# Performance work log

Measured on AMD Instinct MI355X. Metric: run time of the kernel, lower is better.

The kernel has to match this reference:

```python
import jax, jax.numpy as jnp
import numpy as np

B, S, IN_DIM, EMBED, H = 2, 2048, 512, 512, 8
HD = EMBED // H


def setup_inputs() -> dict:
    key = jax.random.key(0)
    ks = jax.random.split(key, 6)
    x = jax.random.normal(ks[0], (B, S, IN_DIM), dtype=jnp.float32)
    dist_mat = jax.random.normal(ks[1], (B, H, S, S), dtype=jnp.float32) * 0.02
    path_mat = jax.random.normal(ks[2], (B, H, S, S), dtype=jnp.float32) * 0.02
    # xavier-uniform-style init scale
    qkv_w = jax.random.normal(ks[3], (IN_DIM, 3 * EMBED), dtype=jnp.float32) * (1.0 / np.sqrt(IN_DIM))
    qkv_b = jnp.zeros((3 * EMBED,), dtype=jnp.float32)
    o_w = jax.random.normal(ks[4], (EMBED, EMBED), dtype=jnp.float32) * (1.0 / np.sqrt(EMBED))
    o_b = jnp.zeros((EMBED,), dtype=jnp.float32)
    return {"x": x, "dist_mat": dist_mat, "path_mat": path_mat,
            "qkv_w": qkv_w, "qkv_b": qkv_b, "o_w": o_w, "o_b": o_b}


def reference(x, dist_mat, path_mat, qkv_w, qkv_b, o_w, o_b):
    b, s, _ = x.shape
    qkv = x @ qkv_w + qkv_b                         # [B,S,3*EMBED]
    qkv = qkv.reshape(b, s, H, 3 * HD).transpose(0, 2, 1, 3)  # [B,H,S,3*HD]
    q, k, v = jnp.split(qkv, 3, axis=-1)            # each [B,H,S,HD]
    logits = jnp.einsum('bhqd,bhkd->bhqk', q, k) / jnp.sqrt(jnp.float32(HD))
    attn = jax.nn.softmax(logits, axis=-1)
    attn = attn + dist_mat + path_mat               # post-softmax bias (breaks flash fusion)
    vals = jnp.einsum('bhqk,bhkd->bhqd', attn, v)   # [B,H,S,HD]
    vals = vals.transpose(0, 2, 1, 3).reshape(b, s, EMBED)
    return vals @ o_w + o_b
```

## Files before the change

kernel.cpp:

```cpp
#include <hip/hip_runtime.h>
#include <stdint.h>
#include <stddef.h>

#define B_ 2
#define H_ 8
#define S_ 2048
#define D_ 64
#define E_ 512
#define N3_ 1536
#define M_ (B_*S_)
#define K_ 512

typedef __attribute__((ext_vector_type(4))) float f32x4;
typedef __attribute__((ext_vector_type(8))) __bf16 bf16x8;
typedef __attribute__((ext_vector_type(4))) __bf16 bf16x4;

static __device__ __forceinline__ int swz(int b) { return b ^ (((b >> 7) & 7) << 4); }

static __device__ __forceinline__ void gl_lds16(const void* g, void* l) {
    __builtin_amdgcn_global_load_lds((const __attribute__((address_space(1))) void*)g,
                                     (__attribute__((address_space(3))) void*)l, 16, 0, 0);
}

__global__ void cvt_bf16_kernel(const float* __restrict__ in, __bf16* __restrict__ out, int n4) {
    int i = blockIdx.x * blockDim.x + threadIdx.x;
    if (i < n4) {
        float4 v = reinterpret_cast<const float4*>(in)[i];
        bf16x4 o;
        o[0] = (__bf16)v.x; o[1] = (__bf16)v.y; o[2] = (__bf16)v.z; o[3] = (__bf16)v.w;
        reinterpret_cast<bf16x4*>(out)[i] = o;
    }
}

__global__ void transpose_cvt_kernel(const float* __restrict__ in, __bf16* __restrict__ out,
                                     int R, int C) {
    __shared__ float tile[32][33];
    int tc = blockIdx.x * 32, tr = blockIdx.y * 32;
    int lx = threadIdx.x & 31, ly = threadIdx.x >> 5;
    #pragma unroll
    for (int p = 0; p < 4; ++p) {
        int r = tr + ly + p * 8, c = tc + lx;
        if (r < R && c < C) tile[ly + p * 8][lx] = in[(size_t)r * C + c];
    }
    __syncthreads();
    #pragma unroll
    for (int p = 0; p < 4; ++p) {
        int oc = tc + ly + p * 8;
        int orow = tr + lx;
        if (oc < C && orow < R) out[(size_t)oc * R + orow] = (__bf16)tile[lx][ly + p * 8];
    }
}

__global__ void transpose_v_kernel(const __bf16* __restrict__ v, __bf16* __restrict__ vt) {
    __shared__ __bf16 t[64][65];
    int bh = blockIdx.x >> 5;
    int s0 = (blockIdx.x & 31) << 6;
    int tid = threadIdx.x;
    const __bf16* src = v + ((size_t)bh * S_ + s0) * D_;
    #pragma unroll
    for (int p = 0; p < 2; ++p) {
        int idx = (p * 256 + tid) * 8;
        int r = idx >> 6, c = idx & 63;
        bf16x8 val = *reinterpret_cast<const bf16x8*>(src + (size_t)r * D_ + c);
        #pragma unroll
        for (int e = 0; e < 8; ++e) t[r][c + e] = val[e];
    }
    __syncthreads();
    __bf16* dst = vt + (size_t)bh * D_ * S_ + s0;
    #pragma unroll
    for (int p = 0; p < 16; ++p) {
        int idx = p * 256 + tid;
        int d = idx >> 6, s = idx & 63;
        dst[(size_t)d * S_ + s] = t[s][d];
    }
}

template<int MODE>
__global__ __launch_bounds__(256, 2) void gemm_kernel(
    const __bf16* __restrict__ A, const __bf16* __restrict__ Bt,
    const float* __restrict__ bias,
    void* __restrict__ o0, void* __restrict__ o1, void* __restrict__ o2,
    int M, int N, int K)
{
    __shared__ __align__(16) __bf16 lA[128 * 64];
    __shared__ __align__(16) __bf16 lB[128 * 64];
    const int tid = threadIdx.x;
    const int wave = tid >> 6, lane = tid & 63;
    const int wm = wave >> 1, wn = wave & 1;
    const int m0 = blockIdx.y * 128, n0 = blockIdx.x * 128;
    const int l15 = lane & 15, l4 = lane >> 4;

    f32x4 acc[4][4] = {};

    for (int k0 = 0; k0 < K; k0 += 64) {
        __syncthreads();
        #pragma unroll
        for (int p = 0; p < 4; ++p) {
            int base = p * 4096 + wave * 1024;
            int js = swz(base + lane * 16);
            int row = js >> 7, colb = js & 127;
            gl_lds16((const char*)A + ((size_t)(m0 + row) * K + k0) * 2 + colb, (char*)lA + base);
            gl_lds16((const char*)Bt + ((size_t)(n0 + row) * K + k0) * 2 + colb, (char*)lB + base);
        }
        __syncthreads();
        #pragma unroll
        for (int ks = 0; ks < 2; ++ks) {
            bf16x8 af[4], bfr[4];
            #pragma unroll
            for (int i = 0; i < 4; ++i) {
                af[i]  = *(const bf16x8*)((const char*)lA + swz(((wm * 64 + i * 16 + l15) << 7) + ks * 64 + (l4 << 4)));
                bfr[i] = *(const bf16x8*)((const char*)lB + swz(((wn * 64 + i * 16 + l15) << 7) + ks * 64 + (l4 << 4)));
            }
            #pragma unroll
            for (int i = 0; i < 4; ++i)
                #pragma unroll
                for (int j = 0; j < 4; ++j)
                    acc[i][j] = __builtin_amdgcn_mfma_f32_16x16x32_bf16(af[i], bfr[j], acc[i][j], 0, 0, 0);
        }
    }
    #pragma unroll
    for (int i = 0; i < 4; ++i) {
        int mg0 = m0 + wm * 64 + i * 16 + (l4 << 2);
        #pragma unroll
        for (int j = 0; j < 4; ++j) {
            int ng = n0 + wn * 64 + j * 16 + l15;
            float bv = bias[ng];
            #pragma unroll
            for (int r = 0; r < 4; ++r) {
                int m = mg0 + r;
                float val = acc[i][j][r] + bv;
                if (MODE == 0) {
                    int h = ng / 192, rr = ng % 192;
                    int which = rr >> 6, d = rr & 63;
                    int b = m >> 11, s = m & (S_ - 1);
                    if (which == 0) val *= 0.125f;
                    __bf16* dst = which == 0 ? (__bf16*)o0 : which == 1 ? (__bf16*)o1 : (__bf16*)o2;
                    dst[(((size_t)((b * H_ + h) * S_ + s)) << 6) + d] = (__bf16)val;
                } else {
                    ((float*)o0)[(size_t)m * N + ng] = val;
                }
            }
        }
    }
}

#define NBIAS 512
__global__ __launch_bounds__(256, 4) void fused_kernel(
    const __bf16* __restrict__ q, const __bf16* __restrict__ k,
    const __bf16* __restrict__ vt,
    const float* __restrict__ dist, const float* __restrict__ path,
    float* __restrict__ attno, float* __restrict__ biaso)
{
    __shared__ __align__(16) __bf16 kl[64 * 64];
    __shared__ __align__(16) __bf16 vl[64 * 64];
    __shared__ __align__(16) __bf16 pl[4][16 * 64];
    const int tid = threadIdx.x, wave = tid >> 6, lane = tid & 63;
    const int l15 = lane & 15, l4 = lane >> 4;
    const int id = blockIdx.x;

    if (id < NBIAS) {
        const int xcd = id & 7, j = id >> 3;
        const int bh = xcd * 2 + (j >> 5), m0 = (j & 31) << 6;
        const int row = m0 + wave * 16 + l15;
        const float* dp = dist + ((size_t)bh * S_ + row) * S_;
        const float* pp = path + ((size_t)bh * S_ + row) * S_;
        const __bf16* vtp = vt + (size_t)bh * D_ * S_;
        f32x4 acc[4] = {};
        #pragma unroll 2
        for (int k0 = 0; k0 < S_; k0 += 32) {
            int kc = k0 + (l4 << 3);
            float4 d0 = *(const float4*)(dp + kc), d1 = *(const float4*)(dp + kc + 4);
            float4 p0 = *(const float4*)(pp + kc), p1 = *(const float4*)(pp + kc + 4);
            bf16x8 a;
            a[0] = (__bf16)(d0.x + p0.x); a[1] = (__bf16)(d0.y + p0.y);
            a[2] = (__bf16)(d0.z + p0.z); a[3] = (__bf16)(d0.w + p0.w);
            a[4] = (__bf16)(d1.x + p1.x); a[5] = (__bf16)(d1.y + p1.y);
            a[6] = (__bf16)(d1.z + p1.z); a[7] = (__bf16)(d1.w + p1.w);
            #pragma unroll
            for (int n = 0; n < 4; ++n) {
                bf16x8 vf = *(const bf16x8*)(vtp + (size_t)(n * 16 + l15) * S_ + kc);
                acc[n] = __builtin_amdgcn_mfma_f32_16x16x32_bf16(a, vf, acc[n], 0, 0, 0);
            }
        }
        #pragma unroll
        for (int n = 0; n < 4; ++n)
            #pragma unroll
            for (int r = 0; r < 4; ++r)
                biaso[((size_t)bh * S_ + m0 + wave * 16 + (l4 << 2) + r) * D_ + n * 16 + l15] = acc[n][r];
        return;
    }

    const int aid = id - NBIAS;
    const int xcd = aid & 7, j = aid >> 3;
    const int bh = xcd * 2 + (j >> 5);
    const int q0 = (j & 31) << 6;
    const int qrow = q0 + wave * 16 + l15;

    const __bf16* qp = q + ((size_t)bh * S_ + qrow) * D_;
    bf16x8 qf0 = *(const bf16x8*)(qp + (l4 << 3));
    bf16x8 qf1 = *(const bf16x8*)(qp + 32 + (l4 << 3));

    float m_run[4], l_run[4];
    f32x4 o_p[4] = {};
    #pragma unroll
    for (int r = 0; r < 4; ++r) { m_run[r] = -1e30f; l_run[r] = 0.f; }

    const char* kg = (const char*)(k + (size_t)bh * S_ * D_);
    const char* vg = (const char*)(vt + (size_t)bh * D_ * S_);

    for (int kt = 0; kt < S_; kt += 64) {
        __syncthreads();
        #pragma unroll
        for (int p = 0; p < 2; ++p) {
            int base = p * 4096 + wave * 1024;
            int js = swz(base + lane * 16);
            int row = js >> 7, colb = js & 127;
            gl_lds16(kg + ((size_t)(kt + row) * D_) * 2 + colb, (char*)kl + base);
            gl_lds16(vg + ((size_t)row * S_ + kt) * 2 + colb, (char*)vl + base);
        }
        __syncthreads();

        f32x4 lg[4] = {};
        #pragma unroll
        for (int ks = 0; ks < 2; ++ks) {
            bf16x8 qa = ks ? qf1 : qf0;
            #pragma unroll
            for (int n = 0; n < 4; ++n) {
                bf16x8 kf = *(const bf16x8*)((const char*)kl + swz(((n * 16 + l15) << 7) + ks * 64 + (l4 << 4)));
                lg[n] = __builtin_amdgcn_mfma_f32_16x16x32_bf16(qa, kf, lg[n], 0, 0, 0);
            }
        }
        float scale[4], rsum[4], pe[4][4];
        #pragma unroll
        for (int r = 0; r < 4; ++r) {
            float t = fmaxf(fmaxf(lg[0][r], lg[1][r]), fmaxf(lg[2][r], lg[3][r]));
            t = fmaxf(t, __shfl_xor(t, 1));
            t = fmaxf(t, __shfl_xor(t, 2));
            t = fmaxf(t, __shfl_xor(t, 4));
            t = fmaxf(t, __shfl_xor(t, 8));
            float mnew = fmaxf(m_run[r], t);
            scale[r] = __expf(m_run[r] - mnew);
            m_run[r] = mnew;
            rsum[r] = 0.f;
        }
        #pragma unroll
        for (int n = 0; n < 4; ++n)
            #pragma unroll
            for (int r = 0; r < 4; ++r) {
                pe[n][r] = __expf(lg[n][r] - m_run[r]);
                rsum[r] += pe[n][r];
            }
        #pragma unroll
        for (int r = 0; r < 4; ++r) {
            float s = rsum[r];
            s += __shfl_xor(s, 1);
            s += __shfl_xor(s, 2);
            s += __shfl_xor(s, 4);
            s += __shfl_xor(s, 8);
            l_run[r] = l_run[r] * scale[r] + s;
        }
        #pragma unroll
        for (int n = 0; n < 4; ++n)
            #pragma unroll
            for (int r = 0; r < 4; ++r)
                o_p[n][r] *= scale[r];
        char* pb = (char*)&pl[wave][0];
        #pragma unroll
        for (int n = 0; n < 4; ++n)
            #pragma unroll
            for (int r = 0; r < 4; ++r) {
                int prow = (l4 << 2) + r, pcol = n * 16 + l15;
                *(__bf16*)(pb + swz((prow << 7) + pcol * 2)) = (__bf16)pe[n][r];
            }
        #pragma unroll
        for (int ks = 0; ks < 2; ++ks) {
            bf16x8 pa = *(const bf16x8*)((const char*)pb + swz((l15 << 7) + ks * 64 + (l4 << 4)));
            #pragma unroll
            for (int n = 0; n < 4; ++n) {
                bf16x8 vf = *(const bf16x8*)((const char*)vl + swz(((n * 16 + l15) << 7) + ks * 64 + (l4 << 4)));
                o_p[n] = __builtin_amdgcn_mfma_f32_16x16x32_bf16(pa, vf, o_p[n], 0, 0, 0);
            }
        }
    }
    #pragma unroll
    for (int r = 0; r < 4; ++r) {
        int s = q0 + wave * 16 + (l4 << 2) + r;
        float inv = 1.f / l_run[r];
        float* dst = attno + ((size_t)bh * S_ + s) * D_;
        #pragma unroll
        for (int n = 0; n < 4; ++n)
            dst[n * 16 + l15] = o_p[n][r] * inv;
    }
}

__global__ void combine_kernel(const float* __restrict__ a, const float* __restrict__ b,
                               __bf16* __restrict__ out) {
    int i = blockIdx.x * blockDim.x + threadIdx.x;
    size_t off = (size_t)i * 8;
    int d = (int)(off & 63);
    int s = (int)((off >> 6) & (S_ - 1));
    int bh = (int)(off >> 17);
    f32x4 a0 = ((const f32x4*)(a + off))[0], a1 = ((const f32x4*)(a + off))[1];
    f32x4 b0 = ((const f32x4*)(b + off))[0], b1 = ((const f32x4*)(b + off))[1];
    bf16x8 o;
    o[0] = (__bf16)(a0[0] + b0[0]); o[1] = (__bf16)(a0[1] + b0[1]);
    o[2] = (__bf16)(a0[2] + b0[2]); o[3] = (__bf16)(a0[3] + b0[3]);
    o[4] = (__bf16)(a1[0] + b1[0]); o[5] = (__bf16)(a1[1] + b1[1]);
    o[6] = (__bf16)(a1[2] + b1[2]); o[7] = (__bf16)(a1[3] + b1[3]);
    int bb = bh >> 3, h = bh & 7;
    *(bf16x8*)(out + ((size_t)(bb * S_ + s) * E_) + h * D_ + d) = o;
}

extern "C" void kernel_launch(void* const* d_in, const int* in_sizes, int n_in,
                              void* d_out, int out_size, void* d_ws, size_t ws_size,
                              hipStream_t stream) {
    (void)in_sizes; (void)n_in; (void)out_size; (void)ws_size;
    const float* x      = (const float*)d_in[0];
    const float* dist   = (const float*)d_in[1];
    const float* path   = (const float*)d_in[2];
    const float* qkv_w  = (const float*)d_in[3];
    const float* qkv_b  = (const float*)d_in[4];
    const float* o_w    = (const float*)d_in[5];
    const float* o_b    = (const float*)d_in[6];
    float* out = (float*)d_out;

    char* ws = (char*)d_ws;
    __bf16* xb     = (__bf16*)(ws);
    __bf16* vb     = (__bf16*)(ws + (4  << 20));
    float*  attno  = (float*) (ws);
    __bf16* qb     = (__bf16*)(ws + (8  << 20));
    __bf16* kb     = (__bf16*)(ws + (12 << 20));
    __bf16* vtb    = (__bf16*)(ws + (16 << 20));
    __bf16* qkv_wT = (__bf16*)(ws + (20 << 20));
    __bf16* o_wT   = (__bf16*)(ws + (20 << 20) + (3 << 19));
    float*  biaso  = (float*) (ws + (22 << 20));
    __bf16* valsb  = (__bf16*)(ws + (30 << 20));

    cvt_bf16_kernel<<<(M_ * K_ / 4 + 255) / 256, 256, 0, stream>>>(x, xb, M_ * K_ / 4);
    transpose_cvt_kernel<<<dim3(N3_ / 32, K_ / 32), 256, 0, stream>>>(qkv_w, qkv_wT, K_, N3_);
    transpose_cvt_kernel<<<dim3(E_ / 32, E_ / 32), 256, 0, stream>>>(o_w, o_wT, E_, E_);
    gemm_kernel<0><<<dim3(N3_ / 128, M_ / 128), 256, 0, stream>>>(xb, qkv_wT, qkv_b, qb, kb, vb, M_, N3_, K_);
    transpose_v_kernel<<<B_ * H_ * (S_ / 64), 256, 0, stream>>>(vb, vtb);
    fused_kernel<<<NBIAS + 512, 256, 0, stream>>>(qb, kb, vtb, dist, path, attno, biaso);
    combine_kernel<<<(B_ * H_ * S_ * D_ / 8) / 256, 256, 0, stream>>>(attno, biaso, valsb);
    gemm_kernel<1><<<dim3(E_ / 128, M_ / 128), 256, 0, stream>>>(valsb, o_wT, o_b, out, nullptr, nullptr, M_, E_, K_);
}
```

Baseline: 228.0 us.

## Double-buffer K/V tiles and interleave bias and attention blocks

The attention path now keeps two LDS buffers for K and V. It prefetches the next 64-key tile with async global-to-LDS loads while it computes the current one, which cuts one barrier per iteration. Bias blocks (streaming dist+path against V) and attention blocks now alternate by block index instead of running as two contiguous ranges, so memory-bound and compute-bound work share the GPU at the same time. The bias loop unroll goes up to 4. The workspace layout is also reshuffled. The extra LDS per block may lower occupancy, and correctness depends on the barrier waiting for the async loads.

```diff
diff --git a/kernel.cpp b/kernel.cpp
--- a/kernel.cpp
+++ b/kernel.cpp
@@ -144,29 +144,30 @@
     }
 }
 
-#define NBIAS 512
 __global__ __launch_bounds__(256, 4) void fused_kernel(
     const __bf16* __restrict__ q, const __bf16* __restrict__ k,
     const __bf16* __restrict__ vt,
     const float* __restrict__ dist, const float* __restrict__ path,
     float* __restrict__ attno, float* __restrict__ biaso)
 {
-    __shared__ __align__(16) __bf16 kl[64 * 64];
-    __shared__ __align__(16) __bf16 vl[64 * 64];
+    __shared__ __align__(16) __bf16 kl[2][64 * 64];
+    __shared__ __align__(16) __bf16 vl[2][64 * 64];
     __shared__ __align__(16) __bf16 pl[4][16 * 64];
     const int tid = threadIdx.x, wave = tid >> 6, lane = tid & 63;
     const int l15 = lane & 15, l4 = lane >> 4;
     const int id = blockIdx.x;
-
-    if (id < NBIAS) {
-        const int xcd = id & 7, j = id >> 3;
-        const int bh = xcd * 2 + (j >> 5), m0 = (j & 31) << 6;
-        const int row = m0 + wave * 16 + l15;
+    const int role = id & 1, sub = id >> 1;
+    const int xcd = sub & 7, jj = sub >> 3;
+    const int bh = xcd * 2 + (jj >> 5);
+    const int q0 = (jj & 31) << 6;
+
+    if (role == 1) {
+        const int row = q0 + wave * 16 + l15;
         const float* dp = dist + ((size_t)bh * S_ + row) * S_;
         const float* pp = path + ((size_t)bh * S_ + row) * S_;
         const __bf16* vtp = vt + (size_t)bh * D_ * S_;
         f32x4 acc[4] = {};
-        #pragma unroll 2
+        #pragma unroll 4
         for (int k0 = 0; k0 < S_; k0 += 32) {
             int kc = k0 + (l4 << 3);
             float4 d0 = *(const float4*)(dp + kc), d1 = *(const float4*)(dp + kc + 4);
@@ -186,39 +187,42 @@
         for (int n = 0; n < 4; ++n)
             #pragma unroll
             for (int r = 0; r < 4; ++r)
-                biaso[((size_t)bh * S_ + m0 + wave * 16 + (l4 << 2) + r) * D_ + n * 16 + l15] = acc[n][r];
+                biaso[((size_t)bh * S_ + q0 + wave * 16 + (l4 << 2) + r) * D_ + n * 16 + l15] = acc[n][r];
         return;
     }
 
-    const int aid = id - NBIAS;
-    const int xcd = aid & 7, j = aid >> 3;
-    const int bh = xcd * 2 + (j >> 5);
-    const int q0 = (j & 31) << 6;
     const int qrow = q0 + wave * 16 + l15;
-
     const __bf16* qp = q + ((size_t)bh * S_ + qrow) * D_;
     bf16x8 qf0 = *(const bf16x8*)(qp + (l4 << 3));
     bf16x8 qf1 = *(const bf16x8*)(qp + 32 + (l4 << 3));
 
-    float m_run[4], l_run[4];
-    f32x4 o_p[4] = {};
-    #pragma unroll
-    for (int r = 0; r < 4; ++r) { m_run[r] = -1e30f; l_run[r] = 0.f; }
-
     const char* kg = (const char*)(k + (size_t)bh * S_ * D_);
     const char* vg = (const char*)(vt + (size_t)bh * D_ * S_);
 
-    for (int kt = 0; kt < S_; kt += 64) {
-        __syncthreads();
+    auto STAGE = [&](int kt, int buf) {
         #pragma unroll
         for (int p = 0; p < 2; ++p) {
             int base = p * 4096 + wave * 1024;
             int js = swz(base + lane * 16);
             int row = js >> 7, colb = js & 127;
-            gl_lds16(kg + ((size_t)(kt + row) * D_) * 2 + colb, (char*)kl + base);
-            gl_lds16(vg + ((size_t)row * S_ + kt) * 2 + colb, (char*)vl + base);
-        }
-        __syncthreads();
+            gl_lds16(kg + ((size_t)(kt + row) * D_) * 2 + colb, (char*)kl[buf] + base);
+            gl_lds16(vg + ((size_t)row * S_ + kt) * 2 + colb, (char*)vl[buf] + base);
+        }
+    };
+
+    float m_run[4], l_run[4];
+    f32x4 o_p[4] = {};
+    #pragma unroll
+    for (int r = 0; r < 4; ++r) { m_run[r] = -1e30f; l_run[r] = 0.f; }
+
+    STAGE(0, 0);
+    __syncthreads();
+
+    int cur = 0;
+    #pragma unroll 1
+    for (int kt = 0; kt < S_; kt += 64) {
+        int ktn = (kt + 64 < S_) ? kt + 64 : kt;
+        STAGE(ktn, cur ^ 1);
 
         f32x4 lg[4] = {};
         #pragma unroll
@@ -226,7 +230,7 @@
             bf16x8 qa = ks ? qf1 : qf0;
             #pragma unroll
             for (int n = 0; n < 4; ++n) {
-                bf16x8 kf = *(const bf16x8*)((const char*)kl + swz(((n * 16 + l15) << 7) + ks * 64 + (l4 << 4)));
+                bf16x8 kf = *(const bf16x8*)((const char*)kl[cur] + swz(((n * 16 + l15) << 7) + ks * 64 + (l4 << 4)));
                 lg[n] = __builtin_amdgcn_mfma_f32_16x16x32_bf16(qa, kf, lg[n], 0, 0, 0);
             }
         }
@@ -277,10 +281,12 @@
             bf16x8 pa = *(const bf16x8*)((const char*)pb + swz((l15 << 7) + ks * 64 + (l4 << 4)));
             #pragma unroll
             for (int n = 0; n < 4; ++n) {
-                bf16x8 vf = *(const bf16x8*)((const char*)vl + swz(((n * 16 + l15) << 7) + ks * 64 + (l4 << 4)));
+                bf16x8 vf = *(const bf16x8*)((const char*)vl[cur] + swz(((n * 16 + l15) << 7) + ks * 64 + (l4 << 4)));
                 o_p[n] = __builtin_amdgcn_mfma_f32_16x16x32_bf16(pa, vf, o_p[n], 0, 0, 0);
             }
         }
+        __syncthreads();
+        cur ^= 1;
     }
     #pragma unroll
     for (int r = 0; r < 4; ++r) {
@@ -293,7 +299,7 @@
     }
 }
 
-__global__ void combine_kernel(const float* __restrict__ a, const float* __restrict__ b,
+__global__ void combine_kernel(const float* __restrict__ a, const float* __restrict__ bsrc,
                                __bf16* __restrict__ out) {
     int i = blockIdx.x * blockDim.x + threadIdx.x;
     size_t off = (size_t)i * 8;
@@ -301,7 +307,7 @@
     int s = (int)((off >> 6) & (S_ - 1));
     int bh = (int)(off >> 17);
     f32x4 a0 = ((const f32x4*)(a + off))[0], a1 = ((const f32x4*)(a + off))[1];
-    f32x4 b0 = ((const f32x4*)(b + off))[0], b1 = ((const f32x4*)(b + off))[1];
+    f32x4 b0 = ((const f32x4*)(bsrc + off))[0], b1 = ((const f32x4*)(bsrc + off))[1];
     bf16x8 o;
     o[0] = (__bf16)(a0[0] + b0[0]); o[1] = (__bf16)(a0[1] + b0[1]);
     o[2] = (__bf16)(a0[2] + b0[2]); o[3] = (__bf16)(a0[3] + b0[3]);
@@ -326,22 +332,22 @@
 
     char* ws = (char*)d_ws;
     __bf16* xb     = (__bf16*)(ws);
-    __bf16* vb     = (__bf16*)(ws + (4  << 20));
-    float*  attno  = (float*) (ws);
-    __bf16* qb     = (__bf16*)(ws + (8  << 20));
-    __bf16* kb     = (__bf16*)(ws + (12 << 20));
-    __bf16* vtb    = (__bf16*)(ws + (16 << 20));
-    __bf16* qkv_wT = (__bf16*)(ws + (20 << 20));
-    __bf16* o_wT   = (__bf16*)(ws + (20 << 20) + (3 << 19));
-    float*  biaso  = (float*) (ws + (22 << 20));
-    __bf16* valsb  = (__bf16*)(ws + (30 << 20));
+    __bf16* valsb  = (__bf16*)(ws);
+    __bf16* qkv_wT = (__bf16*)(ws + (4  << 20));
+    __bf16* o_wT   = (__bf16*)(ws + (4  << 20) + (3 << 19));
+    __bf16* qb     = (__bf16*)(ws + (6  << 20));
+    __bf16* kb     = (__bf16*)(ws + (10 << 20));
+    __bf16* vtb    = (__bf16*)(ws + (14 << 20));
+    __bf16* vb     = (__bf16*)(ws + (18 << 20));
+    float*  attno  = (float*) (ws + (18 << 20));
+    float*  biaso  = (float*) (ws + (26 << 20));
 
     cvt_bf16_kernel<<<(M_ * K_ / 4 + 255) / 256, 256, 0, stream>>>(x, xb, M_ * K_ / 4);
     transpose_cvt_kernel<<<dim3(N3_ / 32, K_ / 32), 256, 0, stream>>>(qkv_w, qkv_wT, K_, N3_);
     transpose_cvt_kernel<<<dim3(E_ / 32, E_ / 32), 256, 0, stream>>>(o_w, o_wT, E_, E_);
     gemm_kernel<0><<<dim3(N3_ / 128, M_ / 128), 256, 0, stream>>>(xb, qkv_wT, qkv_b, qb, kb, vb, M_, N3_, K_);
     transpose_v_kernel<<<B_ * H_ * (S_ / 64), 256, 0, stream>>>(vb, vtb);
-    fused_kernel<<<NBIAS + 512, 256, 0, stream>>>(qb, kb, vtb, dist, path, attno, biaso);
+    fused_kernel<<<1024, 256, 0, stream>>>(qb, kb, vtb, dist, path, attno, biaso);
     combine_kernel<<<(B_ * H_ * S_ * D_ / 8) / 256, 256, 0, stream>>>(attno, biaso, valsb);
     gemm_kernel<1><<<dim3(E_ / 128, M_ / 128), 256, 0, stream>>>(valsb, o_wT, o_b, out, nullptr, nullptr, M_, E_, K_);
 }
```

After: 290.5 us. 1.27x slower.
